# Performance work log

Hardware: AMD Instinct MI355X
Metric: run time of the kernel (lower is better)

## Reference

```python
import jax, jax.numpy as jnp
import numpy as np

OUT_H, OUT_W = 7, 7
SCALE = 0.25
S = 2  # sample_num per bin axis


def _bilinear(img, y, x):
    """Bilinearly sample img[..., H, W] at float coords (y, x).
    y, x have identical shape G; returns img.shape[:-2] + G.
    Matches RoIAlign CUDA interpolation (zero outside [-1, H]/[-1, W])."""
    H, W = img.shape[-2], img.shape[-1]
    valid = (y > -1.0) & (y < H) & (x > -1.0) & (x < W)
    y = jnp.clip(y, 0.0, H - 1)
    x = jnp.clip(x, 0.0, W - 1)
    y0 = jnp.floor(y).astype(jnp.int32)
    x0 = jnp.floor(x).astype(jnp.int32)
    y1 = jnp.minimum(y0 + 1, H - 1)
    x1 = jnp.minimum(x0 + 1, W - 1)
    ly = y - y0
    lx = x - x0
    hy, hx = 1.0 - ly, 1.0 - lx
    v = (hy * hx * img[..., y0, x0] + hy * lx * img[..., y0, x1]
         + ly * hx * img[..., y1, x0] + ly * lx * img[..., y1, x1])
    return jnp.where(valid, v, 0.0)


def setup_inputs() -> dict:
    key = jax.random.key(0)
    k1, k2, k3, k4, k5 = jax.random.split(key, 5)
    N, C, H, W = 2, 256, 200, 200
    R, MH, MW = 512, 128, 128
    features = jax.random.normal(k1, (N, C, H, W), jnp.float32)
    bidx = jax.random.randint(k2, (R,), 0, N)
    xy1 = jax.random.randint(k3, (R, 2), 0, 672)          # x1, y1 (image coords)
    wh = jax.random.randint(k4, (R, 2), 8, 128)           # box sizes in [8,128)
    xy2 = jnp.minimum(xy1 + wh - 1, 799)                  # x2, y2 inclusive
    rois = jnp.concatenate([bidx[:, None].astype(jnp.float32),
                            xy1.astype(jnp.float32),
                            xy2.astype(jnp.float32)], axis=1)  # [R,5]
    batch_masks = jax.random.uniform(k5, (R, MH, MW), jnp.float32)
    # zero-pad beyond each roi's (h, w), mimicking the list->dense packing
    hv = jnp.arange(MH)[None, :] < (xy2[:, 1] - xy1[:, 1] + 1)[:, None]
    wv = jnp.arange(MW)[None, :] < (xy2[:, 0] - xy1[:, 0] + 1)[:, None]
    batch_masks = batch_masks * (hv[:, :, None] & wv[:, None, :]).astype(jnp.float32)
    return {"features": features, "rois": rois, "batch_masks": batch_masks}


def reference(features, rois, batch_masks):
    """Mask-weighted RoIAlign: per-roi bilinear feature samples are weighted by
    the roi's shape mask (bilinearly sampled in roi-relative image coords),
    then average-pooled over the sub-sample grid of each output bin."""
    C = features.shape[1]

    def one_roi(roi, mask):
        b = roi[0].astype(jnp.int32)
        x1, y1, x2, y2 = roi[1], roi[2], roi[3], roi[4]
        roi_start_w = x1 * SCALE
        roi_start_h = y1 * SCALE
        roi_w = jnp.maximum((x2 - x1 + 1.0) * SCALE, 1.0)
        roi_h = jnp.maximum((y2 - y1 + 1.0) * SCALE, 1.0)
        bin_w = roi_w / OUT_W
        bin_h = roi_h / OUT_H
        # sub-sample offsets: (bin + (i+0.5)/S) for i in [0,S)  -> [OUT*S]
        offs = (jnp.arange(S, dtype=jnp.float32) + 0.5) / S
        ys = roi_start_h + (jnp.arange(OUT_H, dtype=jnp.float32)[:, None] + offs[None, :]).reshape(-1) * bin_h
        xs = roi_start_w + (jnp.arange(OUT_W, dtype=jnp.float32)[:, None] + offs[None, :]).reshape(-1) * bin_w
        yy, xx = jnp.meshgrid(ys, xs, indexing='ij')       # [OUT_H*S, OUT_W*S]
        feat = features[b]                                  # [C, H, W]
        vals = _bilinear(feat, yy, xx)                      # [C, OUT_H*S, OUT_W*S]
        # mask weight at the same sample point, in roi-relative image coords
        my = jnp.clip(yy / SCALE - y1, 0.0, y2 - y1)
        mx = jnp.clip(xx / SCALE - x1, 0.0, x2 - x1)
        wgt = _bilinear(mask, my, mx)                       # [OUT_H*S, OUT_W*S]
        v = (vals * wgt).reshape(C, OUT_H, S, OUT_W, S)
        return v.mean(axis=(2, 4))                          # [C, OUT_H, OUT_W]

    return jax.vmap(one_roi)(rois, batch_masks)             # [R, C, OUT_H, OUT_W]
```

## Files before the change

### kernel.cpp

```cpp
#include <hip/hip_runtime.h>


constexpr int   OUT_H = 7, OUT_W = 7;
constexpr int   NBIN  = OUT_H * OUT_W;
constexpr float SCALE = 0.25f;
constexpr int   S     = 2;
constexpr int   NSAMP = NBIN * S * S;
constexpr int   CG16  = 16;
constexpr int   REG   = 34;

typedef unsigned short ushort_t;

__device__ __forceinline__ ushort_t f2bf(float f) {
    unsigned u = __float_as_uint(f);
    u += 0x7fffu + ((u >> 16) & 1u);
    return (ushort_t)(u >> 16);
}
__device__ __forceinline__ float bf2f(ushort_t h) {
    return __uint_as_float(((unsigned)h) << 16);
}
__device__ __forceinline__ unsigned pack2(float a, float b) {
    return (unsigned)f2bf(a) | ((unsigned)f2bf(b) << 16);
}

__global__ __launch_bounds__(256)
void nchw_to_tiled_bf16_kernel(const float* __restrict__ in,
                               ushort_t* __restrict__ out, int C, int P) {
    __shared__ float tile[64][65];
    const int tid = threadIdx.x;
    const int b   = blockIdx.z;
    const int gx  = blockIdx.x * 64;
    const int gy  = blockIdx.y * 64;
    const int NG  = C / CG16;

    const float* inb = in + (size_t)b * C * P;

    {
        const int tx = tid & 15, ty = tid >> 4;
#pragma unroll
        for (int j = 0; j < 4; ++j) {
            const int c_local = ty + 16 * j;
            const float4 v = *(const float4*)&inb[(size_t)(gy + c_local) * P + gx + 4 * tx];
            tile[c_local][4 * tx + 0] = v.x;
            tile[c_local][4 * tx + 1] = v.y;
            tile[c_local][4 * tx + 2] = v.z;
            tile[c_local][4 * tx + 3] = v.w;
        }
    }
    __syncthreads();
    {
        const int gq = tid >> 6;
        const int r  = tid & 63;
        const int g  = (gy >> 4) + gq;
        ushort_t* dstg = out + ((size_t)(b * NG + g) * P) * CG16;
#pragma unroll
        for (int j = 0; j < 2; ++j) {
            const int idx     = r + 64 * j;
            const int p_local = idx >> 1;
            const int half    = idx & 1;
            const int cb      = gq * 16 + half * 8;
            uint4 h;
            h.x = pack2(tile[cb + 0][p_local], tile[cb + 1][p_local]);
            h.y = pack2(tile[cb + 2][p_local], tile[cb + 3][p_local]);
            h.z = pack2(tile[cb + 4][p_local], tile[cb + 5][p_local]);
            h.w = pack2(tile[cb + 6][p_local], tile[cb + 7][p_local]);
            *(uint4*)&dstg[(size_t)(gx + p_local) * CG16 + half * 8] = h;
        }
    }
}

__global__ __launch_bounds__(256)
void mask_roialign_tiled_kernel(const ushort_t* __restrict__ tiled,
                                const float* __restrict__ rois,
                                const float* __restrict__ masks,
                                float*       __restrict__ out,
                                int C, int H, int W, int MH, int MW) {
    __shared__ ushort_t region[REG * REG * CG16];
    __shared__ int      s_off[NSAMP][4];
    __shared__ float    s_w[NSAMP][4];
    __shared__ float    s_outb[CG16 * NBIN];

    const int r   = blockIdx.x;
    const int g   = blockIdx.y;
    const int tid = threadIdx.x;
    const int NG  = C / CG16;

    const float* roi = rois + (size_t)r * 5;
    const int   b  = (int)roi[0];
    const float x1 = roi[1], y1 = roi[2], x2 = roi[3], y2 = roi[4];

    const float roi_start_w = x1 * SCALE;
    const float roi_start_h = y1 * SCALE;
    const float roi_w = fmaxf((x2 - x1 + 1.0f) * SCALE, 1.0f);
    const float roi_h = fmaxf((y2 - y1 + 1.0f) * SCALE, 1.0f);
    const float bin_w = roi_w / (float)OUT_W;
    const float bin_h = roi_h / (float)OUT_H;

    const float xs_min = fminf(fmaxf(roi_start_w + 0.25f * bin_w, 0.0f), (float)(W - 1));
    const float xs_max = fminf(fmaxf(roi_start_w + 6.75f * bin_w, 0.0f), (float)(W - 1));
    const float ys_min = fminf(fmaxf(roi_start_h + 0.25f * bin_h, 0.0f), (float)(H - 1));
    const float ys_max = fminf(fmaxf(roi_start_h + 6.75f * bin_h, 0.0f), (float)(H - 1));
    const int x_lo = (int)floorf(xs_min);
    const int y_lo = (int)floorf(ys_min);
    int x_hi = min((int)floorf(xs_max) + 1, W - 1);
    int y_hi = min((int)floorf(ys_max) + 1, H - 1);
    x_hi = min(x_hi, x_lo + REG - 1);
    y_hi = min(y_hi, y_lo + REG - 1);
    const int cols = x_hi - x_lo + 1;
    const int rows = y_hi - y_lo + 1;

    if (tid < NSAMP) {
        const int bin = tid >> 2;
        const int sub = tid & 3;
        const int ph  = bin / OUT_W, pw = bin % OUT_W;
        const int iy  = sub >> 1,   ix = sub & 1;

        const float yy = roi_start_h + ((float)ph + ((float)iy + 0.5f) * 0.5f) * bin_h;
        const float xx = roi_start_w + ((float)pw + ((float)ix + 0.5f) * 0.5f) * bin_w;

        const bool valid = (yy > -1.0f) && (yy < (float)H) && (xx > -1.0f) && (xx < (float)W);

        const float* msk = masks + (size_t)r * MH * MW;
        float my = fminf(fmaxf(yy * (1.0f / SCALE) - y1, 0.0f), y2 - y1);
        float mx = fminf(fmaxf(xx * (1.0f / SCALE) - x1, 0.0f), x2 - x1);
        my = fminf(fmaxf(my, 0.0f), (float)(MH - 1));
        mx = fminf(fmaxf(mx, 0.0f), (float)(MW - 1));
        const int my0 = (int)floorf(my), mx0 = (int)floorf(mx);
        const int my1 = min(my0 + 1, MH - 1), mx1 = min(mx0 + 1, MW - 1);
        const float mly = my - (float)my0, mlx = mx - (float)mx0;
        const float mhy = 1.0f - mly,      mhx = 1.0f - mlx;
        const float wgt = mhy * mhx * msk[my0 * MW + mx0] + mhy * mlx * msk[my0 * MW + mx1]
                        + mly * mhx * msk[my1 * MW + mx0] + mly * mlx * msk[my1 * MW + mx1];

        const float yc = fminf(fmaxf(yy, 0.0f), (float)(H - 1));
        const float xc = fminf(fmaxf(xx, 0.0f), (float)(W - 1));
        const int y0  = (int)floorf(yc), x0 = (int)floorf(xc);
        const int y1i = min(y0 + 1, H - 1), x1i = min(x0 + 1, W - 1);
        const float ly = yc - (float)y0, lx = xc - (float)x0;
        const float hy = 1.0f - ly,      hx = 1.0f - lx;

        const float scale_all = (valid ? wgt : 0.0f) * (1.0f / (float)(S * S));
        s_w[tid][0] = hy * hx * scale_all;
        s_w[tid][1] = hy * lx * scale_all;
        s_w[tid][2] = ly * hx * scale_all;
        s_w[tid][3] = ly * lx * scale_all;
        const int dy0 = y0 - y_lo, dy1 = y1i - y_lo;
        const int dx0 = x0 - x_lo, dx1 = x1i - x_lo;
        s_off[tid][0] = (dy0 * cols + dx0) * CG16;
        s_off[tid][1] = (dy0 * cols + dx1) * CG16;
        s_off[tid][2] = (dy1 * cols + dx0) * CG16;
        s_off[tid][3] = (dy1 * cols + dx1) * CG16;
    }

    {
        const ushort_t* src = tiled + ((size_t)(b * NG + g) * W * H) * CG16;
        const int cpr   = cols * 2;
        const int total = rows * cpr;
        for (int k = tid; k < total; k += 256) {
            const int ry = k / cpr;
            const int rx = k - ry * cpr;
            const uint4 v = *(const uint4*)&src[((size_t)(y_lo + ry) * W + x_lo) * CG16 + rx * 8];
            *(uint4*)&region[(ry * cols) * CG16 + rx * 8] = v;
        }
    }
    __syncthreads();

    const int cp = tid & 7;
    const int sg = tid >> 3;

    for (int bin = sg; bin < NBIN; bin += 32) {
        float a0 = 0.0f, a1 = 0.0f;
#pragma unroll
        for (int sub = 0; sub < 4; ++sub) {
            const int s = bin * 4 + sub;
            const int   o0 = s_off[s][0], o1 = s_off[s][1], o2 = s_off[s][2], o3 = s_off[s][3];
            const float w0 = s_w[s][0],   w1 = s_w[s][1],   w2 = s_w[s][2],   w3 = s_w[s][3];
            const unsigned u0 = *(const unsigned*)&region[o0 + 2 * cp];
            const unsigned u1 = *(const unsigned*)&region[o1 + 2 * cp];
            const unsigned u2 = *(const unsigned*)&region[o2 + 2 * cp];
            const unsigned u3 = *(const unsigned*)&region[o3 + 2 * cp];
            a0 += w0 * __uint_as_float(u0 << 16) + w1 * __uint_as_float(u1 << 16)
                + w2 * __uint_as_float(u2 << 16) + w3 * __uint_as_float(u3 << 16);
            a1 += w0 * __uint_as_float(u0 & 0xffff0000u) + w1 * __uint_as_float(u1 & 0xffff0000u)
                + w2 * __uint_as_float(u2 & 0xffff0000u) + w3 * __uint_as_float(u3 & 0xffff0000u);
        }
        s_outb[(2 * cp + 0) * NBIN + bin] = a0;
        s_outb[(2 * cp + 1) * NBIN + bin] = a1;
    }
    __syncthreads();

    float* outr = out + ((size_t)r * C + (size_t)g * CG16) * NBIN;
    const float4* s4 = (const float4*)s_outb;
    float4*       o4 = (float4*)outr;
    for (int i = tid; i < (CG16 * NBIN) / 4; i += 256)
        o4[i] = s4[i];
}

__global__ __launch_bounds__(256)
void mask_roialign_kernel(const float* __restrict__ features,
                          const float* __restrict__ rois,
                          const float* __restrict__ masks,
                          float*       __restrict__ out,
                          int C, int H, int W, int MH, int MW) {
    int blk = blockIdx.x;
    int pw  = blk % OUT_W;
    int ph  = (blk / OUT_W) % OUT_H;
    int r   = blk / (OUT_W * OUT_H);
    int c   = threadIdx.x;

    const float* roi = rois + (size_t)r * 5;
    int   b  = (int)roi[0];
    float x1 = roi[1], y1 = roi[2], x2 = roi[3], y2 = roi[4];

    float roi_start_w = x1 * SCALE;
    float roi_start_h = y1 * SCALE;
    float roi_w = fmaxf((x2 - x1 + 1.0f) * SCALE, 1.0f);
    float roi_h = fmaxf((y2 - y1 + 1.0f) * SCALE, 1.0f);
    float bin_w = roi_w / (float)OUT_W;
    float bin_h = roi_h / (float)OUT_H;

    const float* fch = features + ((size_t)b * C + c) * (size_t)(H * W);
    const float* msk = masks + (size_t)r * MH * MW;

    float acc = 0.0f;
#pragma unroll
    for (int iy = 0; iy < S; ++iy) {
        float yy = roi_start_h + ((float)ph + ((float)iy + 0.5f) / (float)S) * bin_h;
#pragma unroll
        for (int ix = 0; ix < S; ++ix) {
            float xx = roi_start_w + ((float)pw + ((float)ix + 0.5f) / (float)S) * bin_w;
            bool valid = (yy > -1.0f) && (yy < (float)H) && (xx > -1.0f) && (xx < (float)W);
            float my = fminf(fmaxf(yy / SCALE - y1, 0.0f), fminf(y2 - y1, (float)(MH - 1)));
            float mx = fminf(fmaxf(xx / SCALE - x1, 0.0f), fminf(x2 - x1, (float)(MW - 1)));
            int my0 = (int)floorf(my), mx0 = (int)floorf(mx);
            int my1 = min(my0 + 1, MH - 1), mx1 = min(mx0 + 1, MW - 1);
            float mly = my - my0, mlx = mx - mx0, mhy = 1.0f - mly, mhx = 1.0f - mlx;
            float wgt = mhy * mhx * msk[my0 * MW + mx0] + mhy * mlx * msk[my0 * MW + mx1]
                      + mly * mhx * msk[my1 * MW + mx0] + mly * mlx * msk[my1 * MW + mx1];
            if (valid) {
                float yc = fminf(fmaxf(yy, 0.0f), (float)(H - 1));
                float xc = fminf(fmaxf(xx, 0.0f), (float)(W - 1));
                int y0 = (int)floorf(yc), x0 = (int)floorf(xc);
                int y1i = min(y0 + 1, H - 1), x1i = min(x0 + 1, W - 1);
                float ly = yc - y0, lx = xc - x0, hy = 1.0f - ly, hx = 1.0f - lx;
                float v = hy * hx * fch[y0  * W + x0 ] + hy * lx * fch[y0  * W + x1i]
                        + ly * hx * fch[y1i * W + x0 ] + ly * lx * fch[y1i * W + x1i];
                acc += wgt * v;
            }
        }
    }
    out[((size_t)r * C + c) * (size_t)NBIN + ph * OUT_W + pw] = acc * (1.0f / (S * S));
}

extern "C" void kernel_launch(void* const* d_in, const int* in_sizes, int n_in,
                              void* d_out, int out_size, void* d_ws, size_t ws_size,
                              hipStream_t stream) {
    const float* features = (const float*)d_in[0];
    const float* rois     = (const float*)d_in[1];
    const float* masks    = (const float*)d_in[2];
    float*       out      = (float*)d_out;

    const int R  = in_sizes[1] / 5;
    const int C  = out_size / (R * NBIN);
    const int H  = 200, W = 200;
    const int MH = 128, MW = 128;
    const int N  = in_sizes[0] / (C * H * W);
    const int P  = H * W;

    const size_t need = (size_t)N * C * P * sizeof(ushort_t);
    const bool tiles_ok = (C % 64 == 0) && (P % 64 == 0);
    if (ws_size >= need && tiles_ok) {
        ushort_t* tiled = (ushort_t*)d_ws;
        dim3 tg(P / 64, C / 64, N);
        nchw_to_tiled_bf16_kernel<<<tg, dim3(256), 0, stream>>>(features, tiled, C, P);

        mask_roialign_tiled_kernel<<<dim3(R, C / CG16), dim3(256), 0, stream>>>(
            tiled, rois, masks, out, C, H, W, MH, MW);
    } else {
        mask_roialign_kernel<<<dim3(R * NBIN), dim3(256), 0, stream>>>(
            features, rois, masks, out, C, H, W, MH, MW);
    }
}
```

Before: 188.5 us.

## Gather bilinear taps directly from global memory and reorder grid by channel group

```diff
diff --git a/kernel.cpp b/kernel.cpp
--- a/kernel.cpp
+++ b/kernel.cpp
@@ -7,7 +7,6 @@
 constexpr int   S     = 2;
 constexpr int   NSAMP = NBIN * S * S;
 constexpr int   CG16  = 16;
-constexpr int   REG   = 34;
 
 typedef unsigned short ushort_t;
 
@@ -70,50 +69,37 @@
 }
 
 __global__ __launch_bounds__(256)
-void mask_roialign_tiled_kernel(const ushort_t* __restrict__ tiled,
-                                const float* __restrict__ rois,
-                                const float* __restrict__ masks,
-                                float*       __restrict__ out,
-                                int C, int H, int W, int MH, int MW) {
-    __shared__ ushort_t region[REG * REG * CG16];
-    __shared__ int      s_off[NSAMP][4];
-    __shared__ float    s_w[NSAMP][4];
-    __shared__ float    s_outb[CG16 * NBIN];
-
-    const int r   = blockIdx.x;
-    const int g   = blockIdx.y;
+void mask_roialign_xcd_kernel(const ushort_t* __restrict__ tiled,
+                              const float* __restrict__ rois,
+                              const float* __restrict__ masks,
+                              float*       __restrict__ out,
+                              int C, int H, int W, int MH, int MW) {
+    __shared__ int   s_off[NSAMP][4];
+    __shared__ float s_w[NSAMP][4];
+    __shared__ float s_outb[CG16 * NBIN];
+
+    const int g   = blockIdx.x;
+    const int r   = blockIdx.y;
     const int tid = threadIdx.x;
     const int NG  = C / CG16;
+    const int P   = H * W;
 
     const float* roi = rois + (size_t)r * 5;
     const int   b  = (int)roi[0];
     const float x1 = roi[1], y1 = roi[2], x2 = roi[3], y2 = roi[4];
-
-    const float roi_start_w = x1 * SCALE;
-    const float roi_start_h = y1 * SCALE;
-    const float roi_w = fmaxf((x2 - x1 + 1.0f) * SCALE, 1.0f);
-    const float roi_h = fmaxf((y2 - y1 + 1.0f) * SCALE, 1.0f);
-    const float bin_w = roi_w / (float)OUT_W;
-    const float bin_h = roi_h / (float)OUT_H;
-
-    const float xs_min = fminf(fmaxf(roi_start_w + 0.25f * bin_w, 0.0f), (float)(W - 1));
-    const float xs_max = fminf(fmaxf(roi_start_w + 6.75f * bin_w, 0.0f), (float)(W - 1));
-    const float ys_min = fminf(fmaxf(roi_start_h + 0.25f * bin_h, 0.0f), (float)(H - 1));
-    const float ys_max = fminf(fmaxf(roi_start_h + 6.75f * bin_h, 0.0f), (float)(H - 1));
-    const int x_lo = (int)floorf(xs_min);
-    const int y_lo = (int)floorf(ys_min);
-    int x_hi = min((int)floorf(xs_max) + 1, W - 1);
-    int y_hi = min((int)floorf(ys_max) + 1, H - 1);
-    x_hi = min(x_hi, x_lo + REG - 1);
-    y_hi = min(y_hi, y_lo + REG - 1);
-    const int cols = x_hi - x_lo + 1;
-    const int rows = y_hi - y_lo + 1;
 
     if (tid < NSAMP) {
         const int bin = tid >> 2;
         const int sub = tid & 3;
         const int ph  = bin / OUT_W, pw = bin % OUT_W;
         const int iy  = sub >> 1,   ix = sub & 1;
+
+        const float roi_start_w = x1 * SCALE;
+        const float roi_start_h = y1 * SCALE;
+        const float roi_w = fmaxf((x2 - x1 + 1.0f) * SCALE, 1.0f);
+        const float roi_h = fmaxf((y2 - y1 + 1.0f) * SCALE, 1.0f);
+        const float bin_w = roi_w / (float)OUT_W;
+        const float bin_h = roi_h / (float)OUT_H;
 
         const float yy = roi_start_h + ((float)ph + ((float)iy + 0.5f) * 0.5f) * bin_h;
         const float xx = roi_start_w + ((float)pw + ((float)ix + 0.5f) * 0.5f) * bin_w;
@@ -144,56 +130,43 @@
         s_w[tid][1] = hy * lx * scale_all;
         s_w[tid][2] = ly * hx * scale_all;
         s_w[tid][3] = ly * lx * scale_all;
-        const int dy0 = y0 - y_lo, dy1 = y1i - y_lo;
-        const int dx0 = x0 - x_lo, dx1 = x1i - x_lo;
-        s_off[tid][0] = (dy0 * cols + dx0) * CG16;
-        s_off[tid][1] = (dy0 * cols + dx1) * CG16;
-        s_off[tid][2] = (dy1 * cols + dx0) * CG16;
-        s_off[tid][3] = (dy1 * cols + dx1) * CG16;
-    }
-
-    {
-        const ushort_t* src = tiled + ((size_t)(b * NG + g) * W * H) * CG16;
-        const int cpr   = cols * 2;
-        const int total = rows * cpr;
-        for (int k = tid; k < total; k += 256) {
-            const int ry = k / cpr;
-            const int rx = k - ry * cpr;
-            const uint4 v = *(const uint4*)&src[((size_t)(y_lo + ry) * W + x_lo) * CG16 + rx * 8];
-            *(uint4*)&region[(ry * cols) * CG16 + rx * 8] = v;
-        }
+        s_off[tid][0] = (y0  * W + x0 ) * CG16;
+        s_off[tid][1] = (y0  * W + x1i) * CG16;
+        s_off[tid][2] = (y1i * W + x0 ) * CG16;
+        s_off[tid][3] = (y1i * W + x1i) * CG16;
     }
     __syncthreads();
 
-    const int cp = tid & 7;
-    const int sg = tid >> 3;
-
-    for (int bin = sg; bin < NBIN; bin += 32) {
-        float a0 = 0.0f, a1 = 0.0f;
+    if (tid < NSAMP) {
+        const int bin = tid >> 2;
+        const int cq  = tid & 3;
+        const ushort_t* gpl = tiled + ((size_t)(b * NG + g) * P) * CG16 + cq * 4;
+
+        float a0 = 0.0f, a1 = 0.0f, a2 = 0.0f, a3 = 0.0f;
 #pragma unroll
         for (int sub = 0; sub < 4; ++sub) {
             const int s = bin * 4 + sub;
-            const int   o0 = s_off[s][0], o1 = s_off[s][1], o2 = s_off[s][2], o3 = s_off[s][3];
-            const float w0 = s_w[s][0],   w1 = s_w[s][1],   w2 = s_w[s][2],   w3 = s_w[s][3];
-            const unsigned u0 = *(const unsigned*)&region[o0 + 2 * cp];
-            const unsigned u1 = *(const unsigned*)&region[o1 + 2 * cp];
-            const unsigned u2 = *(const unsigned*)&region[o2 + 2 * cp];
-            const unsigned u3 = *(const unsigned*)&region[o3 + 2 * cp];
-            a0 += w0 * __uint_as_float(u0 << 16) + w1 * __uint_as_float(u1 << 16)
-                + w2 * __uint_as_float(u2 << 16) + w3 * __uint_as_float(u3 << 16);
-            a1 += w0 * __uint_as_float(u0 & 0xffff0000u) + w1 * __uint_as_float(u1 & 0xffff0000u)
-                + w2 * __uint_as_float(u2 & 0xffff0000u) + w3 * __uint_as_float(u3 & 0xffff0000u);
-        }
-        s_outb[(2 * cp + 0) * NBIN + bin] = a0;
-        s_outb[(2 * cp + 1) * NBIN + bin] = a1;
+#pragma unroll
+            for (int k = 0; k < 4; ++k) {
+                const int   off = s_off[s][k];
+                const float w   = s_w[s][k];
+                const ushort4 q = *(const ushort4*)&gpl[off];
+                a0 += w * bf2f(q.x);
+                a1 += w * bf2f(q.y);
+                a2 += w * bf2f(q.z);
+                a3 += w * bf2f(q.w);
+            }
+        }
+        s_outb[(cq * 4 + 0) * NBIN + bin] = a0;
+        s_outb[(cq * 4 + 1) * NBIN + bin] = a1;
+        s_outb[(cq * 4 + 2) * NBIN + bin] = a2;
+        s_outb[(cq * 4 + 3) * NBIN + bin] = a3;
     }
     __syncthreads();
 
     float* outr = out + ((size_t)r * C + (size_t)g * CG16) * NBIN;
-    const float4* s4 = (const float4*)s_outb;
-    float4*       o4 = (float4*)outr;
-    for (int i = tid; i < (CG16 * NBIN) / 4; i += 256)
-        o4[i] = s4[i];
+    for (int i = tid; i < CG16 * NBIN; i += 256)
+        outr[i] = s_outb[i];
 }
 
 __global__ __launch_bounds__(256)
@@ -274,7 +247,7 @@
         dim3 tg(P / 64, C / 64, N);
         nchw_to_tiled_bf16_kernel<<<tg, dim3(256), 0, stream>>>(features, tiled, C, P);
 
-        mask_roialign_tiled_kernel<<<dim3(R, C / CG16), dim3(256), 0, stream>>>(
+        mask_roialign_xcd_kernel<<<dim3(C / CG16, R), dim3(256), 0, stream>>>(
             tiled, rois, masks, out, C, H, W, MH, MW);
     } else {
         mask_roialign_kernel<<<dim3(R * NBIN), dim3(256), 0, stream>>>(
```

New measurement: 177.3 us. -5.9%, faster.
